# Optimization experiments

Hardware: AMD Instinct MI355X
Metric: run time of the kernel (lower is better)

Reference implementation:

```python
import jax, jax.numpy as jnp
import numpy as np

B, S, D = 2, 2048, 2048
H, KV = 16, 4
HD = D // H          # 128
G = H // KV          # 4
EPS = 1e-5


def _rms_norm(t, w):
    # standard RMSNorm over last dim (intended math of the module's qk norm)
    return t * jax.lax.rsqrt(jnp.mean(t * t, axis=-1, keepdims=True) + EPS) * w


def _rope(t, cos, sin):
    # t: [b, h, s, hd]; cos/sin: [s, hd]
    hd = t.shape[-1]
    t1, t2 = t[..., : hd // 2], t[..., hd // 2 :]
    rot = jnp.concatenate([-t2, t1], axis=-1)
    return t * cos[None, None] + rot * sin[None, None]


def setup_inputs() -> dict:
    key = jax.random.key(0)
    ks = jax.random.split(key, 8)
    x = jax.random.normal(ks[0], (B, S, D), dtype=jnp.float32)
    # causal mask: True = masked out
    mask = jnp.triu(jnp.ones((S, S), dtype=bool), k=1)
    # RoPE tables
    inv_freq = 1.0 / (10000.0 ** (np.arange(0, HD, 2, dtype=np.float32) / HD))
    ang = np.arange(S, dtype=np.float32)[:, None] * inv_freq[None, :]  # [S, HD/2]
    ang = np.concatenate([ang, ang], axis=-1)                          # [S, HD]
    cos = jnp.asarray(np.cos(ang))
    sin = jnp.asarray(np.sin(ang))
    sc = 1.0 / np.sqrt(D)
    W_q = jax.random.normal(ks[1], (D, D), dtype=jnp.float32) * sc
    W_k = jax.random.normal(ks[2], (KV * HD, D), dtype=jnp.float32) * sc
    W_v = jax.random.normal(ks[3], (KV * HD, D), dtype=jnp.float32) * sc
    W_o = jax.random.normal(ks[4], (D, D), dtype=jnp.float32) * sc
    q_norm_w = jnp.ones((HD,), dtype=jnp.float32)
    k_norm_w = jnp.ones((HD,), dtype=jnp.float32)
    return {"x": x, "mask": mask, "cos": cos, "sin": sin,
            "W_q": W_q, "W_k": W_k, "W_v": W_v, "W_o": W_o,
            "q_norm_w": q_norm_w, "k_norm_w": k_norm_w}


def reference(x, mask, cos, sin, W_q, W_k, W_v, W_o, q_norm_w, k_norm_w):
    b, s, d = x.shape
    q = (x @ W_q.T).reshape(b, s, H, HD).transpose(0, 2, 1, 3)   # [b,H,s,hd]
    k = (x @ W_k.T).reshape(b, s, KV, HD).transpose(0, 2, 1, 3)  # [b,KV,s,hd]
    v = (x @ W_v.T).reshape(b, s, KV, HD).transpose(0, 2, 1, 3)
    q = _rms_norm(q, q_norm_w)
    k = _rms_norm(k, k_norm_w)
    q = _rope(q, cos, sin)
    k = _rope(k, cos, sin)
    # GQA: group queries by kv head, avoid materializing expanded K/V
    qg = q.reshape(b, KV, G, s, HD)
    scores = jnp.einsum("bkgqd,bktd->bkgqt", qg, k) / jnp.sqrt(jnp.float32(HD))
    scores = jnp.where(mask[None, None, None], -jnp.inf, scores)
    att = jax.nn.softmax(scores, axis=-1)
    ctx = jnp.einsum("bkgqt,bktd->bkgqd", att, v)
    ctx = ctx.reshape(b, H, s, HD).transpose(0, 2, 1, 3).reshape(b, s, d)
    return ctx @ W_o.T
```

## Files before the change

kernel.cpp:

```cpp
#include <hip/hip_runtime.h>

typedef unsigned short u16;
typedef __bf16 bf16x8 __attribute__((ext_vector_type(8)));
typedef float f32x4 __attribute__((ext_vector_type(4)));
typedef u16 u16x8 __attribute__((ext_vector_type(8)));
typedef u16 u16x4 __attribute__((ext_vector_type(4)));

static constexpr int S_LEN  = 2048;
static constexpr int DMODEL = 2048;
static constexpr int NKV    = 4;
static constexpr int HD     = 128;

__device__ __forceinline__ u16 f2bf(float f) {
  unsigned u = __builtin_bit_cast(unsigned, f);
  u += 0x7fffu + ((u >> 16) & 1u);
  return (u16)(u >> 16);
}
__device__ __forceinline__ float bf2f(u16 h) {
  unsigned u = ((unsigned)h) << 16;
  return __builtin_bit_cast(float, u);
}
__device__ __forceinline__ bf16x8 as_bf(u16x8 v) { return __builtin_bit_cast(bf16x8, v); }

__device__ __forceinline__ u16x8 cvt8(const float* p) {
  f32x4 lo = *(const f32x4*)p;
  f32x4 hi = *(const f32x4*)(p + 4);
  u16x8 r;
#pragma unroll
  for (int j = 0; j < 4; ++j) { r[j] = f2bf(lo[j]); r[j + 4] = f2bf(hi[j]); }
  return r;
}

__device__ __forceinline__ void gld16(const u16* g, u16* l) {
  auto gp = (const __attribute__((address_space(1))) unsigned*)(unsigned long long)g;
  auto lp = (__attribute__((address_space(3))) unsigned*)(unsigned)(unsigned long long)l;
  __builtin_amdgcn_global_load_lds(gp, lp, 16, 0, 0);
}

__global__ __launch_bounds__(256) void cvt_all(
    const float* __restrict__ x,  const float* __restrict__ wq,
    const float* __restrict__ wk, const float* __restrict__ wv,
    const float* __restrict__ wo,
    u16* __restrict__ xb, u16* __restrict__ wall, u16* __restrict__ wob)
{
  const long i = (long)blockIdx.x * 256 + threadIdx.x;
  const float* src; u16* dst; long j, o;
  if (i < 1048576)      { src = x;  dst = xb;   j = i;           o = i; }
  else if (i < 1572864) { src = wq; dst = wall; j = i - 1048576; o = i - 1048576; }
  else if (i < 1703936) { src = wk; dst = wall; j = i - 1572864; o = i - 1048576; }
  else if (i < 1835008) { src = wv; dst = wall; j = i - 1703936; o = i - 1048576; }
  else                  { src = wo; dst = wob;  j = i - 1835008; o = i - 1835008; }
  *(u16x8*)(dst + o * 8) = cvt8(src + j * 8);
}

__global__ __launch_bounds__(256) void gemm_qkv(
    const u16* __restrict__ A, const u16* __restrict__ Bw,
    u16* __restrict__ Cq, u16* __restrict__ Ck, u16* __restrict__ Cv)
{
  constexpr int K = 2048;
  __shared__ u16 As[128 * 64];
  __shared__ u16 Bs[128 * 64];
  const int bx = blockIdx.x;
  const int bm = bx / 24, bn = bx % 24;
  const int tid = threadIdx.x, wave = tid >> 6, lane = tid & 63;
  const int wm = (wave & 1) << 6, wn = (wave >> 1) << 6;
  const long m0 = (long)bm << 7, n0 = (long)bn << 7;

  f32x4 acc[4][4] = {};

  const int srow = (wave << 5) + (lane >> 3);
  const int sch  = ((lane & 7) ^ ((lane >> 3) & 7)) << 3;
  const u16* ga = A  + (m0 + srow) * K + sch;
  const u16* gb = Bw + (n0 + srow) * K + sch;
  u16* la = As + (wave << 11);
  u16* lb = Bs + (wave << 11);
  const long rstep = (long)8 * K;

  const int fr = lane & 15, fhi = lane >> 4;

  for (int k0 = 0; k0 < K; k0 += 64) {
    __syncthreads();
#pragma unroll
    for (int i = 0; i < 4; ++i) {
      gld16(ga + k0 + i * rstep, la + i * 512);
      gld16(gb + k0 + i * rstep, lb + i * 512);
    }
    __syncthreads();
#pragma unroll
    for (int kb = 0; kb < 2; ++kb) {
      bf16x8 af[4], bf[4];
#pragma unroll
      for (int i = 0; i < 4; ++i) {
        const int row = wm + (i << 4) + fr;
        const int cc  = (((kb << 2) + fhi) ^ (fr & 7)) << 3;
        af[i] = as_bf(*(const u16x8*)&As[row * 64 + cc]);
      }
#pragma unroll
      for (int i = 0; i < 4; ++i) {
        const int row = wn + (i << 4) + fr;
        const int cc  = (((kb << 2) + fhi) ^ (fr & 7)) << 3;
        bf[i] = as_bf(*(const u16x8*)&Bs[row * 64 + cc]);
      }
#pragma unroll
      for (int mi = 0; mi < 4; ++mi)
#pragma unroll
        for (int ni = 0; ni < 4; ++ni)
          acc[mi][ni] = __builtin_amdgcn_mfma_f32_16x16x32_bf16(af[mi], bf[ni], acc[mi][ni], 0, 0, 0);
    }
  }

  u16* Cb; int N2; long c0;
  if (bn < 16)      { Cb = Cq; N2 = 2048; c0 = n0; }
  else if (bn < 20) { Cb = Ck; N2 = 512;  c0 = n0 - 2048; }
  else              { Cb = Cv; N2 = 512;  c0 = n0 - 2560; }

  const int er = (lane >> 4) << 2, ec = lane & 15;
#pragma unroll
  for (int mi = 0; mi < 4; ++mi)
#pragma unroll
    for (int ni = 0; ni < 4; ++ni) {
      u16* cp = Cb + (m0 + wm + (mi << 4) + er) * N2 + (c0 + wn + (ni << 4) + ec);
#pragma unroll
      for (int r = 0; r < 4; ++r)
        cp[(long)r * N2] = f2bf(acc[mi][ni][r]);
    }
}

__global__ __launch_bounds__(256) void gemm_o(
    const u16* __restrict__ A, const u16* __restrict__ Bw, float* __restrict__ C)
{
  constexpr int K = 2048, N = 2048;
  __shared__ u16 As[128 * 64];
  __shared__ u16 Bs[128 * 64];
  const int bx = blockIdx.x;
  const int bm = bx >> 4, bn = bx & 15;
  const int tid = threadIdx.x, wave = tid >> 6, lane = tid & 63;
  const int wm = (wave & 1) << 6, wn = (wave >> 1) << 6;
  const long m0 = (long)bm << 7, n0 = (long)bn << 7;

  f32x4 acc[4][4] = {};

  const int srow = (wave << 5) + (lane >> 3);
  const int sch  = ((lane & 7) ^ ((lane >> 3) & 7)) << 3;
  const u16* ga = A  + (m0 + srow) * K + sch;
  const u16* gb = Bw + (n0 + srow) * K + sch;
  u16* la = As + (wave << 11);
  u16* lb = Bs + (wave << 11);
  const long rstep = (long)8 * K;

  const int fr = lane & 15, fhi = lane >> 4;

  for (int k0 = 0; k0 < K; k0 += 64) {
    __syncthreads();
#pragma unroll
    for (int i = 0; i < 4; ++i) {
      gld16(ga + k0 + i * rstep, la + i * 512);
      gld16(gb + k0 + i * rstep, lb + i * 512);
    }
    __syncthreads();
#pragma unroll
    for (int kb = 0; kb < 2; ++kb) {
      bf16x8 af[4], bf[4];
#pragma unroll
      for (int i = 0; i < 4; ++i) {
        const int cc = (((kb << 2) + fhi) ^ (fr & 7)) << 3;
        af[i] = as_bf(*(const u16x8*)&As[(wm + (i << 4) + fr) * 64 + cc]);
        bf[i] = as_bf(*(const u16x8*)&Bs[(wn + (i << 4) + fr) * 64 + cc]);
      }
#pragma unroll
      for (int mi = 0; mi < 4; ++mi)
#pragma unroll
        for (int ni = 0; ni < 4; ++ni)
          acc[mi][ni] = __builtin_amdgcn_mfma_f32_16x16x32_bf16(af[mi], bf[ni], acc[mi][ni], 0, 0, 0);
    }
  }

  const int er = (lane >> 4) << 2, ec = lane & 15;
#pragma unroll
  for (int mi = 0; mi < 4; ++mi)
#pragma unroll
    for (int ni = 0; ni < 4; ++ni) {
      float* cp = C + (m0 + wm + (mi << 4) + er) * N + (n0 + wn + (ni << 4) + ec);
#pragma unroll
      for (int r = 0; r < 4; ++r)
        cp[(long)r * N] = acc[mi][ni][r];
    }
}

__global__ __launch_bounds__(256) void k_prep(
    u16* __restrict__ kb, const float* __restrict__ kw,
    const float* __restrict__ cosb, const float* __restrict__ sinb,
    const u16* __restrict__ v, u16* __restrict__ vt)
{
  const int bx = blockIdx.x;
  if (bx < 4096) {
    const int row  = bx * 4 + (threadIdx.x >> 6);
    const int lane = threadIdx.x & 63;
    const int s = (row >> 2) & (S_LEN - 1);
    u16* p = kb + (long)row * HD;
    float t1 = bf2f(p[lane]), t2 = bf2f(p[lane + 64]);
    float ss = t1 * t1 + t2 * t2;
#pragma unroll
    for (int off = 32; off; off >>= 1) ss += __shfl_xor(ss, off);
    const float r = rsqrtf(ss * (1.0f / 128.0f) + 1e-5f);
    t1 *= r * kw[lane];
    t2 *= r * kw[lane + 64];
    const float* cp = cosb + s * HD;
    const float* sp = sinb + s * HD;
    p[lane]      = f2bf(t1 * cp[lane]      - t2 * sp[lane]);
    p[lane + 64] = f2bf(t2 * cp[lane + 64] + t1 * sp[lane + 64]);
  } else {
    const int idx = (bx - 4096) * 256 + threadIdx.x;
    const int t0  = (idx & 255) << 3;
    const int hd0 = ((idx >> 8) & 15) << 3;
    const int bkv = idx >> 12;
    const u16* vp = v + ((long)(bkv >> 2) * S_LEN + t0) * 512 + ((bkv & 3) << 7) + hd0;
    u16x8 rw[8];
#pragma unroll
    for (int c = 0; c < 8; ++c) rw[c] = *(const u16x8*)(vp + (long)c * 512);
    u16* op = vt + ((long)bkv * HD + hd0) * S_LEN + t0;
#pragma unroll
    for (int j = 0; j < 8; ++j) {
      u16x8 o;
#pragma unroll
      for (int c = 0; c < 8; ++c) o[c] = rw[c][j];
      *(u16x8*)(op + (long)j * S_LEN) = o;
    }
  }
}

__global__ __launch_bounds__(256, 2) void flash(
    const u16* __restrict__ q, const u16* __restrict__ k,
    const u16* __restrict__ vt, u16* __restrict__ ctx,
    const float* __restrict__ qw,
    const float* __restrict__ cosb, const float* __restrict__ sinb)
{
  __shared__ u16 Ks[128 * 128];
  __shared__ u16 Vs[128 * 128];
  const int tid = threadIdx.x, wave = tid >> 6, lane = tid & 63;
  const int bx  = blockIdx.x;
  const int qtr = bx & 15;
  const int bh  = bx >> 4;
  const int qt  = (bx < 256) ? (15 - qtr) : qtr;
  const int b   = bh >> 4, h = bh & 15;
  const int kv  = h >> 2;
  const int q0  = qt << 7;

  const int fr = lane & 15, fhi = lane >> 4;

  bf16x8 qf[2][4];
#pragma unroll
  for (int nq = 0; nq < 2; ++nq) {
    const int srow = q0 + (wave << 5) + (nq << 4) + fr;
    const u16* qp = q + ((long)b * S_LEN + srow) * DMODEL + h * HD;
    float qv[4][8];
    float ss = 0.f;
#pragma unroll
    for (int kb = 0; kb < 4; ++kb) {
      u16x8 raw = *(const u16x8*)(qp + (kb << 5) + (fhi << 3));
#pragma unroll
      for (int j = 0; j < 8; ++j) {
        const float v = bf2f(raw[j]);
        qv[kb][j] = v;
        ss += v * v;
      }
    }
    ss += __shfl_xor(ss, 16);
    ss += __shfl_xor(ss, 32);
    const float rn = rsqrtf(ss * (1.0f / 128.0f) + 1e-5f);
    const float* cp = cosb + srow * HD;
    const float* sp = sinb + srow * HD;
#pragma unroll
    for (int kb = 0; kb < 4; ++kb) {
      u16x8 pk;
#pragma unroll
      for (int j = 0; j < 8; ++j) {
        const int kk = (kb << 5) + (fhi << 3) + j;
        const float tk = qv[kb][j]     * rn * qw[kk];
        const float tp = qv[kb ^ 2][j] * rn * qw[kk ^ 64];
        const float o = (tk * cp[kk] + ((kb < 2) ? -tp : tp) * sp[kk])
                        * 0.08838834764831845f;
        pk[j] = f2bf(o);
      }
      qf[nq][kb] = as_bf(pk);
    }
  }

  f32x4 O[8][2] = {};
  float lS[2] = {0.f, 0.f};

  const u16* kbase = k + ((long)b * S_LEN) * 512 + kv * HD;
  const u16* vbase = vt + ((long)(b * NKV + kv)) * HD * S_LEN;

  for (int jt = 0; jt <= qt; ++jt) {
    const int t0 = jt << 7;
    __syncthreads();
#pragma unroll
    for (int i = 0; i < 8; ++i) {
      const int row = (wave << 5) + (i << 2) + fhi;
      const int gc  = fr ^ (row & 15);
      gld16(kbase + (long)(t0 + row) * 512 + (gc << 3),
            Ks + (((wave << 5) + (i << 2)) << 7));
      gld16(vbase + (long)row * S_LEN + t0 + (gc << 3),
            Vs + (((wave << 5) + (i << 2)) << 7));
    }
    __syncthreads();

    f32x4 Sac[8][2] = {};
#pragma unroll
    for (int mt = 0; mt < 8; ++mt) {
      const int t = (mt << 4) + fr;
      bf16x8 kf[4];
#pragma unroll
      for (int kb = 0; kb < 4; ++kb) {
        const int cc = ((kb << 2) + fhi) ^ (t & 15);
        kf[kb] = as_bf(*(const u16x8*)&Ks[t * 128 + (cc << 3)]);
      }
#pragma unroll
      for (int nq = 0; nq < 2; ++nq)
#pragma unroll
        for (int kb = 0; kb < 4; ++kb)
          Sac[mt][nq] = __builtin_amdgcn_mfma_f32_16x16x32_bf16(kf[kb], qf[nq][kb], Sac[mt][nq], 0, 0, 0);
    }

    if (jt == qt) {
#pragma unroll
      for (int mt = 0; mt < 8; ++mt)
#pragma unroll
        for (int nq = 0; nq < 2; ++nq) {
          const int qin = (wave << 5) + (nq << 4) + fr;
#pragma unroll
          for (int r = 0; r < 4; ++r)
            if ((mt << 4) + (fhi << 2) + r > qin) Sac[mt][nq][r] = -1e30f;
        }
    }

#pragma unroll
    for (int nq = 0; nq < 2; ++nq) {
      float rsum = 0.f;
#pragma unroll
      for (int mt = 0; mt < 8; ++mt)
#pragma unroll
        for (int r = 0; r < 4; ++r) {
          const float e = __expf(Sac[mt][nq][r]);
          Sac[mt][nq][r] = e;
          rsum += e;
        }
      rsum += __shfl_xor(rsum, 16);
      rsum += __shfl_xor(rsum, 32);
      lS[nq] += rsum;
    }

    __syncthreads();

#pragma unroll
    for (int nq = 0; nq < 2; ++nq) {
      const int qrow = (wave << 5) + (nq << 4) + fr;
#pragma unroll
      for (int mt = 0; mt < 8; ++mt) {
        u16x4 pk;
#pragma unroll
        for (int r = 0; r < 4; ++r) pk[r] = f2bf(Sac[mt][nq][r]);
        const int cs = ((mt << 1) + (fhi >> 1)) ^ (fr & 7);
        *(u16x4*)&Ks[qrow * 128 + (cs << 3) + ((fhi & 1) << 2)] = pk;
      }
    }
    asm volatile("" ::: "memory");

    bf16x8 pf[2][4];
#pragma unroll
    for (int nq = 0; nq < 2; ++nq) {
      const int qrow = (wave << 5) + (nq << 4) + fr;
#pragma unroll
      for (int kt = 0; kt < 4; ++kt) {
        const int cs = ((kt << 2) + fhi) ^ (fr & 7);
        pf[nq][kt] = as_bf(*(const u16x8*)&Ks[qrow * 128 + (cs << 3)]);
      }
    }
#pragma unroll
    for (int mh = 0; mh < 8; ++mh) {
      const int hd = (mh << 4) + fr;
      bf16x8 vf[4];
#pragma unroll
      for (int kt = 0; kt < 4; ++kt) {
        const int cc = ((kt << 2) + fhi) ^ (hd & 15);
        vf[kt] = as_bf(*(const u16x8*)&Vs[hd * 128 + (cc << 3)]);
      }
#pragma unroll
      for (int nq = 0; nq < 2; ++nq)
#pragma unroll
        for (int kt = 0; kt < 4; ++kt)
          O[mh][nq] = __builtin_amdgcn_mfma_f32_16x16x32_bf16(vf[kt], pf[nq][kt], O[mh][nq], 0, 0, 0);
    }
  }

#pragma unroll
  for (int nq = 0; nq < 2; ++nq) {
    const float inv = 1.0f / lS[nq];
    const long s = q0 + (wave << 5) + (nq << 4) + fr;
    u16* cp = ctx + ((long)b * S_LEN + s) * DMODEL + h * HD;
#pragma unroll
    for (int mh = 0; mh < 8; ++mh) {
      u16x4 pk;
#pragma unroll
      for (int r = 0; r < 4; ++r) pk[r] = f2bf(O[mh][nq][r] * inv);
      *(u16x4*)(cp + (mh << 4) + (fhi << 2)) = pk;
    }
  }
}

extern "C" void kernel_launch(void* const* d_in, const int* in_sizes, int n_in,
                              void* d_out, int out_size, void* d_ws, size_t ws_size,
                              hipStream_t stream) {
  const float* x    = (const float*)d_in[0];
  const float* cosb = (const float*)d_in[2];
  const float* sinb = (const float*)d_in[3];
  const float* Wq   = (const float*)d_in[4];
  const float* Wk   = (const float*)d_in[5];
  const float* Wv   = (const float*)d_in[6];
  const float* Wo   = (const float*)d_in[7];
  const float* qw   = (const float*)d_in[8];
  const float* kw   = (const float*)d_in[9];

  u16* qb  = (u16*)d_out;
  u16* xb  = qb + 8388608;
  u16* kb   = (u16*)d_ws;
  u16* vb   = kb  + 2097152;
  u16* vtb  = vb  + 2097152;
  u16* ctx  = vtb + 2097152;
  u16* wall = ctx;
  u16* wob  = ctx + 8388608;
  float* out = (float*)d_out;

  cvt_all<<<dim3(9216), dim3(256), 0, stream>>>(x, Wq, Wk, Wv, Wo, xb, wall, wob);
  gemm_qkv<<<dim3(768), dim3(256), 0, stream>>>(xb, wall, qb, kb, vb);
  k_prep<<<dim3(4224), dim3(256), 0, stream>>>(kb, kw, cosb, sinb, vb, vtb);
  flash<<<dim3(512), dim3(256), 0, stream>>>(qb, kb, vtb, ctx, qw, cosb, sinb);
  gemm_o<<<dim3(512), dim3(256), 0, stream>>>(ctx, wob, out);
}
```

Before: 327.1 us.

## Share one LDS tile for K and V and shuffle P via registers

The flash-attention kernel now uses a single 32KB LDS buffer instead of separate K and V buffers. V is loaded only after QK^T and softmax are done, and it overwrites the K tile. The P matrix is rearranged into MFMA operand layout with cross-lane shuffles instead of a round trip through LDS. Launch bounds rise to 3 blocks per CU to use the freed LDS. The cost is that the V load is now serialized after the score computation, which adds load latency on every tile, plus extra shuffle instructions and more register pressure under the tighter occupancy bound.

```diff
diff --git a/kernel.cpp b/kernel.cpp
--- a/kernel.cpp
+++ b/kernel.cpp
@@ -5,6 +5,7 @@
 typedef float f32x4 __attribute__((ext_vector_type(4)));
 typedef u16 u16x8 __attribute__((ext_vector_type(8)));
 typedef u16 u16x4 __attribute__((ext_vector_type(4)));
+typedef unsigned u32x4 __attribute__((ext_vector_type(4)));
 
 static constexpr int S_LEN  = 2048;
 static constexpr int DMODEL = 2048;
@@ -229,14 +230,13 @@
   }
 }
 
-__global__ __launch_bounds__(256, 2) void flash(
+__global__ __launch_bounds__(256, 3) void flash(
     const u16* __restrict__ q, const u16* __restrict__ k,
     const u16* __restrict__ vt, u16* __restrict__ ctx,
     const float* __restrict__ qw,
     const float* __restrict__ cosb, const float* __restrict__ sinb)
 {
-  __shared__ u16 Ks[128 * 128];
-  __shared__ u16 Vs[128 * 128];
+  __shared__ u16 Ts[128 * 128];
   const int tid = threadIdx.x, wave = tid >> 6, lane = tid & 63;
   const int bx  = blockIdx.x;
   const int qtr = bx & 15;
@@ -292,6 +292,10 @@
   const u16* kbase = k + ((long)b * S_LEN) * 512 + kv * HD;
   const u16* vbase = vt + ((long)(b * NKV + kv)) * HD * S_LEN;
 
+  const int s0 = fr + ((fhi & 1) << 5);
+  const int s1 = s0 + 16;
+  const int selhi = fhi >> 1;
+
   for (int jt = 0; jt <= qt; ++jt) {
     const int t0 = jt << 7;
     __syncthreads();
@@ -300,9 +304,7 @@
       const int row = (wave << 5) + (i << 2) + fhi;
       const int gc  = fr ^ (row & 15);
       gld16(kbase + (long)(t0 + row) * 512 + (gc << 3),
-            Ks + (((wave << 5) + (i << 2)) << 7));
-      gld16(vbase + (long)row * S_LEN + t0 + (gc << 3),
-            Vs + (((wave << 5) + (i << 2)) << 7));
+            Ts + (((wave << 5) + (i << 2)) << 7));
     }
     __syncthreads();
 
@@ -314,7 +316,7 @@
 #pragma unroll
       for (int kb = 0; kb < 4; ++kb) {
         const int cc = ((kb << 2) + fhi) ^ (t & 15);
-        kf[kb] = as_bf(*(const u16x8*)&Ks[t * 128 + (cc << 3)]);
+        kf[kb] = as_bf(*(const u16x8*)&Ts[t * 128 + (cc << 3)]);
       }
 #pragma unroll
       for (int nq = 0; nq < 2; ++nq)
@@ -335,48 +337,58 @@
         }
     }
 
+    unsigned p01[8][2], p23[8][2];
 #pragma unroll
     for (int nq = 0; nq < 2; ++nq) {
       float rsum = 0.f;
 #pragma unroll
-      for (int mt = 0; mt < 8; ++mt)
+      for (int mt = 0; mt < 8; ++mt) {
 #pragma unroll
         for (int r = 0; r < 4; ++r) {
           const float e = __expf(Sac[mt][nq][r]);
           Sac[mt][nq][r] = e;
           rsum += e;
         }
+        p01[mt][nq] = (unsigned)f2bf(Sac[mt][nq][0]) | ((unsigned)f2bf(Sac[mt][nq][1]) << 16);
+        p23[mt][nq] = (unsigned)f2bf(Sac[mt][nq][2]) | ((unsigned)f2bf(Sac[mt][nq][3]) << 16);
+      }
       rsum += __shfl_xor(rsum, 16);
       rsum += __shfl_xor(rsum, 32);
       lS[nq] += rsum;
     }
 
     __syncthreads();
-
-#pragma unroll
-    for (int nq = 0; nq < 2; ++nq) {
-      const int qrow = (wave << 5) + (nq << 4) + fr;
-#pragma unroll
-      for (int mt = 0; mt < 8; ++mt) {
-        u16x4 pk;
-#pragma unroll
-        for (int r = 0; r < 4; ++r) pk[r] = f2bf(Sac[mt][nq][r]);
-        const int cs = ((mt << 1) + (fhi >> 1)) ^ (fr & 7);
-        *(u16x4*)&Ks[qrow * 128 + (cs << 3) + ((fhi & 1) << 2)] = pk;
-      }
-    }
-    asm volatile("" ::: "memory");
+#pragma unroll
+    for (int i = 0; i < 8; ++i) {
+      const int row = (wave << 5) + (i << 2) + fhi;
+      const int gc  = fr ^ (row & 15);
+      gld16(vbase + (long)row * S_LEN + t0 + (gc << 3),
+            Ts + (((wave << 5) + (i << 2)) << 7));
+    }
 
     bf16x8 pf[2][4];
 #pragma unroll
-    for (int nq = 0; nq < 2; ++nq) {
-      const int qrow = (wave << 5) + (nq << 4) + fr;
+    for (int nq = 0; nq < 2; ++nq)
 #pragma unroll
       for (int kt = 0; kt < 4; ++kt) {
-        const int cs = ((kt << 2) + fhi) ^ (fr & 7);
-        pf[nq][kt] = as_bf(*(const u16x8*)&Ks[qrow * 128 + (cs << 3)]);
-      }
-    }
+        const int mA = kt << 1, mB = mA + 1;
+        const unsigned a0 = __shfl(p01[mA][nq], s0);
+        const unsigned b0 = __shfl(p01[mB][nq], s0);
+        const unsigned a1 = __shfl(p23[mA][nq], s0);
+        const unsigned b1 = __shfl(p23[mB][nq], s0);
+        const unsigned a2 = __shfl(p01[mA][nq], s1);
+        const unsigned b2 = __shfl(p01[mB][nq], s1);
+        const unsigned a3 = __shfl(p23[mA][nq], s1);
+        const unsigned b3 = __shfl(p23[mB][nq], s1);
+        u32x4 w;
+        w[0] = selhi ? b0 : a0;
+        w[1] = selhi ? b1 : a1;
+        w[2] = selhi ? b2 : a2;
+        w[3] = selhi ? b3 : a3;
+        pf[nq][kt] = as_bf(__builtin_bit_cast(u16x8, w));
+      }
+    __syncthreads();
+
 #pragma unroll
     for (int mh = 0; mh < 8; ++mh) {
       const int hd = (mh << 4) + fr;
@@ -384,7 +396,7 @@
 #pragma unroll
       for (int kt = 0; kt < 4; ++kt) {
         const int cc = ((kt << 2) + fhi) ^ (hd & 15);
-        vf[kt] = as_bf(*(const u16x8*)&Vs[hd * 128 + (cc << 3)]);
+        vf[kt] = as_bf(*(const u16x8*)&Ts[hd * 128 + (cc << 3)]);
       }
 #pragma unroll
       for (int nq = 0; nq < 2; ++nq)
```

After: 412.3 us. +26.1%, slower.
